# Kernel tuning notes

Measured on AMD Instinct MI355X. Metric: run time of the kernel, lower is better.

## Reference

```python
import jax, jax.numpy as jnp
import numpy as np

N_NODES = 30000
N_EDGES = 150000
N_REL = 10
IN_DIM = 256
OUT_DIM = 256


def setup_inputs() -> dict:
    key = jax.random.key(0)
    ks = jax.random.split(key, 10)
    s = 1.0 / np.sqrt(IN_DIM)  # ~nn.Linear init scale
    return {
        "x": jax.random.normal(ks[0], (N_NODES, IN_DIM), jnp.float32),
        "W_self": jax.random.uniform(ks[1], (IN_DIM, OUT_DIM), jnp.float32, -s, s),
        "b_self": jax.random.uniform(ks[2], (OUT_DIM,), jnp.float32, -s, s),
        "W_fwd": jax.random.uniform(ks[3], (N_REL, IN_DIM, OUT_DIM), jnp.float32, -s, s),
        "b_fwd": jax.random.uniform(ks[4], (N_REL, OUT_DIM), jnp.float32, -s, s),
        "W_rev": jax.random.uniform(ks[5], (N_REL, IN_DIM, OUT_DIM), jnp.float32, -s, s),
        "b_rev": jax.random.uniform(ks[6], (N_REL, OUT_DIM), jnp.float32, -s, s),
        "dep_idx": jax.random.randint(ks[7], (N_EDGES,), 0, N_NODES, jnp.int32),
        "rel_idx": jax.random.randint(ks[8], (N_EDGES,), 0, N_REL, jnp.int32),
        "gov_idx": jax.random.randint(ks[9], (N_EDGES,), 0, N_NODES, jnp.int32),
    }


def reference(x, W_self, b_self, W_fwd, b_fwd, W_rev, b_rev, dep_idx, rel_idx, gov_idx):
    # self transform for every token: [N, out]
    out = x @ W_self + b_self
    # transform all nodes by every relation weight up-front: [R, N, out]
    H_fwd = jnp.einsum("ni,rio->rno", x, W_fwd) + b_fwd[:, None, :]
    H_rev = jnp.einsum("ni,rio->rno", x, W_rev) + b_rev[:, None, :]
    # per-edge gather: forward msg uses governor feature, reverse msg uses dependent
    msg_fwd = H_fwd[rel_idx, gov_idx]  # [E, out]
    msg_rev = H_rev[rel_idx, dep_idx]  # [E, out]
    # scatter-add: forward msg -> dependent, reverse msg -> governor
    out = out.at[dep_idx].add(msg_fwd)
    out = out.at[gov_idx].add(msg_rev)
    return out
```

## Files before the change

kernel.cpp:

```cpp
#include <hip/hip_runtime.h>

#define N_NODES 30000
#define N_EDGES 150000
#define N_REL 10
#define DIM 256

#define SORT_BLOCKS 120
#define SORT_CHUNK ((N_EDGES + SORT_BLOCKS - 1) / SORT_BLOCKS)

#define SCAN_CHUNK 256
#define SCAN_BLOCKS ((N_NODES + SCAN_CHUNK - 1) / SCAN_CHUNK)

#define A_STRIDE 280

#define PREP_XB 7500
#define PREP_WB 5376
#define PREP_ZB 235

typedef __attribute__((ext_vector_type(8))) short bf16x8;
typedef __attribute__((ext_vector_type(4))) float f32x4;

__device__ __forceinline__ unsigned short f2bf(float f) {
  union { float f; unsigned int u; } v; v.f = f;
  unsigned int u = v.u;
  unsigned int r = u + 0x7fffu + ((u >> 16) & 1u);
  return (unsigned short)(r >> 16);
}


__global__ void prep_kernel(const float* __restrict__ x,
                            const float* __restrict__ Wf,
                            const float* __restrict__ Wr,
                            const float* __restrict__ Ws,
                            unsigned short* __restrict__ xbf,
                            unsigned short* __restrict__ wt,
                            int* __restrict__ cnt) {
  int b = blockIdx.x;
  if (b < PREP_XB) {
    int idx = b * 256 + threadIdx.x;
    float4 v = reinterpret_cast<const float4*>(x)[idx];
    ushort4 o;
    o.x = f2bf(v.x); o.y = f2bf(v.y); o.z = f2bf(v.z); o.w = f2bf(v.w);
    reinterpret_cast<ushort4*>(xbf)[idx] = o;
  } else if (b < PREP_XB + PREP_WB) {
    int idx = (b - PREP_XB) * 256 + threadIdx.x;
    int bb = idx >> 16;
    int t = idx & 65535;
    int o = t >> 8, i = t & 255;
    const float* src = (bb < N_REL) ? (Wf + (size_t)bb * 65536)
                     : (bb < 2 * N_REL) ? (Wr + (size_t)(bb - N_REL) * 65536)
                     : Ws;
    wt[idx] = f2bf(src[i * 256 + o]);
  } else {
    int i = (b - PREP_XB - PREP_WB) * 256 + threadIdx.x;
    if (i < 2 * N_NODES) cnt[i] = 0;
  }
}

__global__ void hist_all_kernel(const int* __restrict__ rel,
                                const int* __restrict__ dep,
                                const int* __restrict__ gov,
                                int* __restrict__ block_counts,
                                int* __restrict__ cnt) {
  __shared__ int h[N_REL];
  if (threadIdx.x < N_REL) h[threadIdx.x] = 0;
  __syncthreads();
  int beg = blockIdx.x * SORT_CHUNK;
  int end = min(beg + SORT_CHUNK, N_EDGES);
  for (int e = beg + threadIdx.x; e < end; e += blockDim.x) {
    atomicAdd(&h[rel[e]], 1);
    atomicAdd(&cnt[dep[e]], 1);
    atomicAdd(&cnt[N_NODES + gov[e]], 1);
  }
  __syncthreads();
  if (threadIdx.x < N_REL)
    block_counts[blockIdx.x * N_REL + threadIdx.x] = h[threadIdx.x];
}

__global__ void scan_rel_kernel(const int* __restrict__ block_counts,
                                int* __restrict__ rel_start,
                                int* __restrict__ block_offset) {
  __shared__ int tot[N_REL];
  int r = threadIdx.x;
  if (r < N_REL) {
    int s = 0;
    for (int b = 0; b < SORT_BLOCKS; ++b) s += block_counts[b * N_REL + r];
    tot[r] = s;
  }
  __syncthreads();
  if (threadIdx.x == 0) {
    int s = 0;
    for (int i = 0; i < N_REL; ++i) { rel_start[i] = s; s += tot[i]; }
    rel_start[N_REL] = s;
  }
  __syncthreads();
  if (r < N_REL) {
    int run = rel_start[r];
    for (int b = 0; b < SORT_BLOCKS; ++b) {
      block_offset[b * N_REL + r] = run;
      run += block_counts[b * N_REL + r];
    }
  }
}

__global__ void scanA_kernel(const int* __restrict__ cnt,
                             int* __restrict__ tmp, int* __restrict__ sums) {
  __shared__ int s[SCAN_CHUNK];
  int d = blockIdx.y, b = blockIdx.x, t = threadIdx.x;
  int i = b * SCAN_CHUNK + t;
  int v = (i < N_NODES) ? cnt[d * N_NODES + i] : 0;
  s[t] = v;
  __syncthreads();
  for (int off = 1; off < SCAN_CHUNK; off <<= 1) {
    int add = (t >= off) ? s[t - off] : 0;
    __syncthreads();
    s[t] += add;
    __syncthreads();
  }
  if (i < N_NODES) tmp[d * N_NODES + i] = s[t] - v;
  if (t == SCAN_CHUNK - 1) sums[d * SCAN_BLOCKS + b] = s[t];
}

__global__ void scanB_kernel(const int* __restrict__ sums,
                             int* __restrict__ chunk_off, int* __restrict__ rp) {
  __shared__ int s[128];
  int d = blockIdx.x, t = threadIdx.x;
  int v = (t < SCAN_BLOCKS) ? sums[d * SCAN_BLOCKS + t] : 0;
  s[t] = v;
  __syncthreads();
  for (int off = 1; off < 128; off <<= 1) {
    int add = (t >= off) ? s[t - off] : 0;
    __syncthreads();
    s[t] += add;
    __syncthreads();
  }
  if (t < SCAN_BLOCKS) chunk_off[d * SCAN_BLOCKS + t] = s[t] - v;
  if (t == 127) rp[d * (N_NODES + 1) + N_NODES] = s[127];
}

__global__ void scanC_kernel(const int* __restrict__ tmp,
                             const int* __restrict__ chunk_off,
                             int* __restrict__ rp, int* __restrict__ cursor) {
  int d = blockIdx.y;
  int i = blockIdx.x * SCAN_CHUNK + threadIdx.x;
  if (i < N_NODES) {
    int v = tmp[d * N_NODES + i] + chunk_off[d * SCAN_BLOCKS + blockIdx.x];
    rp[d * (N_NODES + 1) + i] = v;
    cursor[d * N_NODES + i] = v;
  }
}

__global__ void scatter_all_kernel(const int* __restrict__ rel,
                                   const int* __restrict__ dep,
                                   const int* __restrict__ gov,
                                   const int* __restrict__ block_offset,
                                   int* __restrict__ cursor,
                                   int* __restrict__ perm,
                                   int* __restrict__ srcf,
                                   int* __restrict__ srcr,
                                   int* __restrict__ colf,
                                   int* __restrict__ colr) {
  __shared__ int cur[N_REL];
  if (threadIdx.x < N_REL)
    cur[threadIdx.x] = block_offset[blockIdx.x * N_REL + threadIdx.x];
  __syncthreads();
  int beg = blockIdx.x * SORT_CHUNK;
  int end = min(beg + SORT_CHUNK, N_EDGES);
  for (int e = beg + threadIdx.x; e < end; e += blockDim.x) {
    int dp = dep[e], gv = gov[e];
    int pos = atomicAdd(&cur[rel[e]], 1);
    perm[pos] = e;
    srcf[pos] = gv;
    srcr[pos] = dp;
    colf[atomicAdd(&cursor[dp], 1)] = pos;
    colr[atomicAdd(&cursor[N_NODES + gv], 1)] = pos;
  }
}


__global__ __launch_bounds__(256, 2)
void mega_gemm_kernel(const unsigned short* __restrict__ xbf,
                      const unsigned short* __restrict__ wt,
                      const float* __restrict__ b_self,
                      const float* __restrict__ b_fwd,
                      const float* __restrict__ b_rev,
                      const int* __restrict__ srcf,
                      const int* __restrict__ srcr,
                      const int* __restrict__ rel_start,
                      unsigned short* __restrict__ msg,
                      float* __restrict__ out) {
  const int bkt = blockIdx.y;
  const bool is_self = (bkt >= 2 * N_REL);
  const bool fwd = bkt < N_REL;
  const int r = is_self ? 0 : (fwd ? bkt : bkt - N_REL);

  int beg, cnt;
  const int* src_arr = fwd ? srcf : srcr;
  unsigned short* mdir = msg + (fwd ? 0 : (size_t)N_EDGES * DIM);
  if (is_self) {
    beg = (bkt - 2 * N_REL) * (N_NODES / 2);
    cnt = N_NODES / 2;
  } else {
    beg = rel_start[r];
    cnt = rel_start[r + 1] - beg;
  }
  const int ntiles = (cnt + 63) >> 6;
  const int GX = gridDim.x;

  const int tid = threadIdx.x;
  const int wave = tid >> 6, lane = tid & 63;
  const int lm = lane & 15, q = lane >> 4;
  const int nb = wave * 64;
  const int half = lane >> 5;
  const int lcol = lane & 31;

  __shared__ int s_src[64];
  __shared__ unsigned short sA[64 * A_STRIDE];

  bf16x8 wf[8][4];
  const unsigned short* wbase = wt + (size_t)(is_self ? 2 * N_REL : bkt) * DIM * DIM;
  #pragma unroll
  for (int kk = 0; kk < 8; ++kk)
    #pragma unroll
    for (int ni = 0; ni < 4; ++ni)
      wf[kk][ni] = *reinterpret_cast<const bf16x8*>(
          wbase + (size_t)(nb + ni * 16 + lm) * DIM + kk * 32 + q * 8);

  const float* bptr = is_self ? b_self : ((fwd ? b_fwd : b_rev) + r * DIM);
  float bias[4];
  #pragma unroll
  for (int ni = 0; ni < 4; ++ni) bias[ni] = bptr[nb + ni * 16 + lm];

  int t = blockIdx.x;
  if (t >= ntiles) return;

  auto load_idx = [&](int tt) -> int {
    int tile0_ = tt << 6;
    if (is_self) {
      int rr = beg + tile0_ + tid;
      return rr < beg + cnt ? rr : beg + cnt - 1;
    } else {
      int p_ = tile0_ + tid;
      p_ = p_ < cnt ? p_ : cnt - 1;
      return src_arr[beg + p_];
    }
  };
  auto issue_D = [&](uint4* d) {
    #pragma unroll
    for (int i = 0; i < 8; ++i) {
      int row = wave * 16 + i * 2 + half;
      d[i] = *reinterpret_cast<const uint4*>(
          xbf + (size_t)s_src[row] * DIM + lcol * 8);
    }
  };
  auto write_A = [&](const uint4* d) {
    #pragma unroll
    for (int i = 0; i < 8; ++i) {
      int row = wave * 16 + i * 2 + half;
      *reinterpret_cast<uint4*>(sA + row * A_STRIDE + lcol * 8) = d[i];
    }
  };

  int idxreg = 0;
  if (tid < 64) s_src[tid] = load_idx(t);
  __syncthreads();
  uint4 d[8];
  issue_D(d);
  if (tid < 64 && t + GX < ntiles) idxreg = load_idx(t + GX);

  for (; t < ntiles; t += GX) {
    const int tile0 = t << 6;
    const int rows_valid = min(64, cnt - tile0);
    const bool have_next = (t + GX) < ntiles;
    const bool have_next2 = (t + 2 * GX) < ntiles;

    __syncthreads();
    if (tid < 64 && have_next) s_src[tid] = idxreg;
    write_A(d);
    if (tid < 64 && have_next2) idxreg = load_idx(t + 2 * GX);
    __syncthreads();
    if (have_next) issue_D(d);

    f32x4 acc[4][4];
    #pragma unroll
    for (int mi = 0; mi < 4; ++mi)
      #pragma unroll
      for (int ni = 0; ni < 4; ++ni)
        acc[mi][ni] = (f32x4){0.f, 0.f, 0.f, 0.f};

    #pragma unroll
    for (int kk = 0; kk < 8; ++kk) {
      bf16x8 a[4];
      #pragma unroll
      for (int mi = 0; mi < 4; ++mi)
        a[mi] = *reinterpret_cast<const bf16x8*>(
            sA + (mi * 16 + lm) * A_STRIDE + kk * 32 + q * 8);
      #pragma unroll
      for (int mi = 0; mi < 4; ++mi)
        #pragma unroll
        for (int ni = 0; ni < 4; ++ni)
          acc[mi][ni] = __builtin_amdgcn_mfma_f32_16x16x32_bf16(a[mi], wf[kk][ni], acc[mi][ni], 0, 0, 0);
    }

    if (is_self) {
      #pragma unroll
      for (int mi = 0; mi < 4; ++mi) {
        #pragma unroll
        for (int reg = 0; reg < 4; ++reg) {
          int row = mi * 16 + q * 4 + reg;
          if (row < rows_valid) {
            #pragma unroll
            for (int ni = 0; ni < 4; ++ni)
              out[(size_t)(beg + tile0 + row) * DIM + nb + ni * 16 + lm] =
                  acc[mi][ni][reg] + bias[ni];
          }
        }
      }
    } else {
      #pragma unroll
      for (int mi = 0; mi < 4; ++mi) {
        #pragma unroll
        for (int reg = 0; reg < 4; ++reg) {
          int row = mi * 16 + q * 4 + reg;
          if (row < rows_valid) {
            unsigned int p0 = ((unsigned int)f2bf(acc[mi][1][reg] + bias[1]) << 16) |
                              f2bf(acc[mi][0][reg] + bias[0]);
            unsigned int p1 = ((unsigned int)f2bf(acc[mi][3][reg] + bias[3]) << 16) |
                              f2bf(acc[mi][2][reg] + bias[2]);
            uint2 u; u.x = p0; u.y = p1;
            *reinterpret_cast<uint2*>(
                mdir + (size_t)(beg + tile0 + row) * DIM + nb + lm * 4) = u;
          }
        }
      }
    }
  }
}


__global__ void reduce_both_kernel(const unsigned short* __restrict__ msg,
                                   const int* __restrict__ rp,
                                   const int* __restrict__ colf,
                                   const int* __restrict__ colr,
                                   float* __restrict__ out) {
  const int n = blockIdx.x, t = threadIdx.x;
  const int g = t >> 6, lane = t & 63;
  const int b0 = rp[n], e0 = rp[n + 1];
  const int b1 = rp[(N_NODES + 1) + n], e1 = rp[(N_NODES + 1) + n + 1];
  if (e0 <= b0 && e1 <= b1) return;

  float a0 = 0.f, a1 = 0.f, a2 = 0.f, a3 = 0.f;
  for (int j = b0 + g; j < e0; j += 4) {
    int row = colf[j];
    uint2 v = *reinterpret_cast<const uint2*>(msg + (size_t)row * DIM + lane * 4);
    union { unsigned int u; float f; } c;
    c.u = v.x << 16;          a0 += c.f;
    c.u = v.x & 0xffff0000u;  a1 += c.f;
    c.u = v.y << 16;          a2 += c.f;
    c.u = v.y & 0xffff0000u;  a3 += c.f;
  }
  for (int j = b1 + g; j < e1; j += 4) {
    int row = colr[j];
    uint2 v = *reinterpret_cast<const uint2*>(
        msg + (size_t)(N_EDGES + row) * DIM + lane * 4);
    union { unsigned int u; float f; } c;
    c.u = v.x << 16;          a0 += c.f;
    c.u = v.x & 0xffff0000u;  a1 += c.f;
    c.u = v.y << 16;          a2 += c.f;
    c.u = v.y & 0xffff0000u;  a3 += c.f;
  }

  __shared__ float part[4][DIM];
  const int cb = (lane >> 4) * 64 + (lane & 15);
  part[g][cb +  0] = a0;
  part[g][cb + 16] = a1;
  part[g][cb + 32] = a2;
  part[g][cb + 48] = a3;
  __syncthreads();
  float s = part[0][t] + part[1][t] + part[2][t] + part[3][t];
  out[(size_t)n * DIM + t] += s;
}


__global__ __launch_bounds__(256, 2)
void self_gemm_kernel(const unsigned short* __restrict__ xbf,
                      const unsigned short* __restrict__ wt_self,
                      const float* __restrict__ b_self,
                      float* __restrict__ out) {
  const int tid = threadIdx.x;
  const int wave = tid >> 6, lane = tid & 63;
  const int lm = lane & 15, q = lane >> 4;
  const int nb = wave * 64;

  bf16x8 wf[8][4];
  #pragma unroll
  for (int kk = 0; kk < 8; ++kk)
    #pragma unroll
    for (int ni = 0; ni < 4; ++ni)
      wf[kk][ni] = *reinterpret_cast<const bf16x8*>(
          wt_self + (size_t)(nb + ni * 16 + lm) * DIM + kk * 32 + q * 8);

  float bias[4];
  #pragma unroll
  for (int ni = 0; ni < 4; ++ni) bias[ni] = b_self[nb + ni * 16 + lm];

  const int ntiles = (N_NODES + 63) / 64;
  for (int t = blockIdx.x; t < ntiles; t += gridDim.x) {
    const int row0 = t * 64;
    const unsigned short* xr[4];
    #pragma unroll
    for (int mi = 0; mi < 4; ++mi) {
      int r = row0 + mi * 16 + lm;
      int rc = r < N_NODES ? r : N_NODES - 1;
      xr[mi] = xbf + (size_t)rc * DIM + q * 8;
    }

    f32x4 acc[4][4];
    #pragma unroll
    for (int mi = 0; mi < 4; ++mi)
      #pragma unroll
      for (int ni = 0; ni < 4; ++ni)
        acc[mi][ni] = (f32x4){0.f, 0.f, 0.f, 0.f};

    #pragma unroll
    for (int kk = 0; kk < 8; ++kk) {
      bf16x8 a[4];
      #pragma unroll
      for (int mi = 0; mi < 4; ++mi)
        a[mi] = *reinterpret_cast<const bf16x8*>(xr[mi] + kk * 32);
      #pragma unroll
      for (int mi = 0; mi < 4; ++mi)
        #pragma unroll
        for (int ni = 0; ni < 4; ++ni)
          acc[mi][ni] = __builtin_amdgcn_mfma_f32_16x16x32_bf16(a[mi], wf[kk][ni], acc[mi][ni], 0, 0, 0);
    }

    #pragma unroll
    for (int mi = 0; mi < 4; ++mi) {
      #pragma unroll
      for (int reg = 0; reg < 4; ++reg) {
        int row = row0 + mi * 16 + q * 4 + reg;
        if (row < N_NODES) {
          #pragma unroll
          for (int ni = 0; ni < 4; ++ni)
            out[(size_t)row * DIM + nb + ni * 16 + lm] = acc[mi][ni][reg] + bias[ni];
        }
      }
    }
  }
}

__global__ void edge_gemm_atomic_kernel(const unsigned short* __restrict__ xbf,
                                        const unsigned short* __restrict__ wt,
                                        const float* __restrict__ b_fwd,
                                        const float* __restrict__ b_rev,
                                        const int* __restrict__ perm,
                                        const int* __restrict__ rel_start,
                                        const int* __restrict__ dep,
                                        const int* __restrict__ gov,
                                        float* __restrict__ out) {
  const int bucket = blockIdx.y;
  const int r = bucket % N_REL;
  const bool fwd = bucket < N_REL;
  const int beg = rel_start[r];
  const int cnt = rel_start[r + 1] - beg;
  const int ntiles = (cnt + 63) >> 6;

  const int tid = threadIdx.x;
  const int wave = tid >> 6, lane = tid & 63;
  const int lm = lane & 15, q = lane >> 4;
  const int nb = wave * 64;

  __shared__ int s_src[64], s_dst[64];

  const unsigned short* wr[4];
  #pragma unroll
  for (int ni = 0; ni < 4; ++ni)
    wr[ni] = wt + (size_t)bucket * DIM * DIM + (size_t)(nb + ni * 16 + lm) * DIM + q * 8;

  const float* bptr = (fwd ? b_fwd : b_rev) + r * DIM;
  float bias[4];
  #pragma unroll
  for (int ni = 0; ni < 4; ++ni) bias[ni] = bptr[nb + ni * 16 + lm];

  for (int t = blockIdx.x; t < ntiles; t += gridDim.x) {
    const int tile0 = t << 6;
    const int rows_valid = min(64, cnt - tile0);

    if (tid < 64) {
      int s = 0, d = -1;
      if (tid < rows_valid) {
        int e = perm[beg + tile0 + tid];
        int gv = gov[e], dp = dep[e];
        s = fwd ? gv : dp;
        d = fwd ? dp : gv;
      }
      s_src[tid] = s;
      s_dst[tid] = d;
    }
    __syncthreads();

    const unsigned short* xr[4];
    #pragma unroll
    for (int mi = 0; mi < 4; ++mi)
      xr[mi] = xbf + (size_t)s_src[mi * 16 + lm] * DIM + q * 8;

    f32x4 acc[4][4];
    #pragma unroll
    for (int mi = 0; mi < 4; ++mi)
      #pragma unroll
      for (int ni = 0; ni < 4; ++ni)
        acc[mi][ni] = (f32x4){0.f, 0.f, 0.f, 0.f};

    #pragma unroll
    for (int k0 = 0; k0 < DIM; k0 += 32) {
      bf16x8 a[4], b[4];
      #pragma unroll
      for (int mi = 0; mi < 4; ++mi) a[mi] = *reinterpret_cast<const bf16x8*>(xr[mi] + k0);
      #pragma unroll
      for (int ni = 0; ni < 4; ++ni) b[ni] = *reinterpret_cast<const bf16x8*>(wr[ni] + k0);
      #pragma unroll
      for (int mi = 0; mi < 4; ++mi)
        #pragma unroll
        for (int ni = 0; ni < 4; ++ni)
          acc[mi][ni] = __builtin_amdgcn_mfma_f32_16x16x32_bf16(a[mi], b[ni], acc[mi][ni], 0, 0, 0);
    }

    #pragma unroll
    for (int mi = 0; mi < 4; ++mi) {
      #pragma unroll
      for (int reg = 0; reg < 4; ++reg) {
        int row = mi * 16 + q * 4 + reg;
        if (row < rows_valid) {
          int dst = s_dst[row];
          float* op = out + (size_t)dst * DIM + nb + lm;
          #pragma unroll
          for (int ni = 0; ni < 4; ++ni)
            atomicAdd(op + ni * 16, acc[mi][ni][reg] + bias[ni]);
        }
      }
    }
    __syncthreads();
  }
}


extern "C" void kernel_launch(void* const* d_in, const int* in_sizes, int n_in,
                              void* d_out, int out_size, void* d_ws, size_t ws_size,
                              hipStream_t stream) {
  const float* x      = (const float*)d_in[0];
  const float* W_self = (const float*)d_in[1];
  const float* b_self = (const float*)d_in[2];
  const float* W_fwd  = (const float*)d_in[3];
  const float* b_fwd  = (const float*)d_in[4];
  const float* W_rev  = (const float*)d_in[5];
  const float* b_rev  = (const float*)d_in[6];
  const int* dep = (const int*)d_in[7];
  const int* rel = (const int*)d_in[8];
  const int* gov = (const int*)d_in[9];
  float* out = (float*)d_out;

  char* base = (char*)d_ws;
  size_t off = 0;
  auto alloc = [&](size_t bytes) -> char* {
    char* p = base + off;
    off = (off + bytes + 15) & ~(size_t)15;
    return p;
  };

  unsigned short* xbf = (unsigned short*)alloc((size_t)N_NODES * DIM * 2);
  unsigned short* wt  = (unsigned short*)alloc((size_t)21 * DIM * DIM * 2);
  int* perm          = (int*)alloc((size_t)N_EDGES * 4);
  int* srcf          = (int*)alloc((size_t)N_EDGES * 4);
  int* srcr          = (int*)alloc((size_t)N_EDGES * 4);
  int* rel_start     = (int*)alloc(16 * 4);
  int* block_counts  = (int*)alloc(SORT_BLOCKS * N_REL * 4);
  int* block_offset  = (int*)alloc(SORT_BLOCKS * N_REL * 4);
  int* cnt       = (int*)alloc((size_t)2 * N_NODES * 4);
  int* tmp       = (int*)alloc((size_t)2 * N_NODES * 4);
  int* sums      = (int*)alloc((size_t)2 * SCAN_BLOCKS * 4);
  int* chunk_off = (int*)alloc((size_t)2 * SCAN_BLOCKS * 4);
  int* rp        = (int*)alloc((size_t)2 * (N_NODES + 1) * 4);
  int* cursor    = (int*)alloc((size_t)2 * N_NODES * 4);
  int* colf      = (int*)alloc((size_t)N_EDGES * 4);
  int* colr      = (int*)alloc((size_t)N_EDGES * 4);
  unsigned short* msg = (unsigned short*)alloc((size_t)2 * N_EDGES * DIM * 2);
  const bool two_phase = (off <= ws_size);

  prep_kernel<<<PREP_XB + PREP_WB + PREP_ZB, 256, 0, stream>>>(
      x, W_fwd, W_rev, W_self, xbf, wt, cnt);
  hist_all_kernel<<<SORT_BLOCKS, 256, 0, stream>>>(rel, dep, gov, block_counts, cnt);
  scan_rel_kernel<<<1, 64, 0, stream>>>(block_counts, rel_start, block_offset);
  scanA_kernel<<<dim3(SCAN_BLOCKS, 2), SCAN_CHUNK, 0, stream>>>(cnt, tmp, sums);
  scanB_kernel<<<2, 128, 0, stream>>>(sums, chunk_off, rp);
  scanC_kernel<<<dim3(SCAN_BLOCKS, 2), SCAN_CHUNK, 0, stream>>>(tmp, chunk_off, rp, cursor);
  scatter_all_kernel<<<SORT_BLOCKS, 256, 0, stream>>>(
      rel, dep, gov, block_offset, cursor, perm, srcf, srcr, colf, colr);

  if (two_phase) {
    mega_gemm_kernel<<<dim3(48, 2 * N_REL + 2), 256, 0, stream>>>(
        xbf, wt, b_self, b_fwd, b_rev, srcf, srcr, rel_start, msg, out);
    reduce_both_kernel<<<N_NODES, 256, 0, stream>>>(msg, rp, colf, colr, out);
  } else {
    self_gemm_kernel<<<120, 256, 0, stream>>>(
        xbf, wt + (size_t)20 * DIM * DIM, b_self, out);
    edge_gemm_atomic_kernel<<<dim3(260, 20), 256, 0, stream>>>(
        xbf, wt, b_fwd, b_rev, perm, rel_start, dep, gov, out);
  }
}
```

Measured before the change: 323.7 us.

## Stream gathered rows straight into double-buffered swizzled LDS with global_load_lds

The gather of node feature rows into shared memory no longer passes through registers and a padded LDS tile. Rows are now loaded directly into LDS with global_load_lds, into a double-buffered tile using an XOR swizzle in place of padding to avoid bank conflicts. Staging of the next tile overlaps the MFMA work on the current one, and there is one fewer barrier per tile and fewer live registers. In exchange LDS use grows to about 64KB per block, which can lower occupancy, and correctness depends on the barrier waiting for the asynchronous LDS loads to finish.

```diff
diff --git a/kernel.cpp b/kernel.cpp
--- a/kernel.cpp
+++ b/kernel.cpp
@@ -10,8 +10,6 @@
 
 #define SCAN_CHUNK 256
 #define SCAN_BLOCKS ((N_NODES + SCAN_CHUNK - 1) / SCAN_CHUNK)
-
-#define A_STRIDE 280
 
 #define PREP_XB 7500
 #define PREP_WB 5376
@@ -212,13 +210,13 @@
   const int lm = lane & 15, q = lane >> 4;
   const int nb = wave * 64;
   const int half = lane >> 5;
-  const int lcol = lane & 31;
-
-  __shared__ int s_src[64];
-  __shared__ unsigned short sA[64 * A_STRIDE];
+
+  __shared__ int s_src[2][64];
+  __shared__ unsigned short sA[2][64 * DIM];
 
   bf16x8 wf[8][4];
-  const unsigned short* wbase = wt + (size_t)(is_self ? 2 * N_REL : bkt) * DIM * DIM;
+  const unsigned short* wbase =
+      wt + (size_t)(is_self ? 2 * N_REL : bkt) * DIM * DIM;
   #pragma unroll
   for (int kk = 0; kk < 8; ++kk)
     #pragma unroll
@@ -230,6 +228,18 @@
   float bias[4];
   #pragma unroll
   for (int ni = 0; ni < 4; ++ni) bias[ni] = bptr[nb + ni * 16 + lm];
+
+  int swz[8];
+  #pragma unroll
+  for (int i = 0; i < 8; ++i)
+    swz[i] = (((lane & 31) ^ ((i * 2 + half) & 7)) * 8);
+  int rowoff[4];
+  #pragma unroll
+  for (int mi = 0; mi < 4; ++mi) rowoff[mi] = (mi * 16 + lm) * DIM;
+  int ckoff[8];
+  #pragma unroll
+  for (int kk = 0; kk < 8; ++kk)
+    ckoff[kk] = ((kk * 4 + q) ^ (lm & 7)) * 8;
 
   int t = blockIdx.x;
   if (t >= ntiles) return;
@@ -245,41 +255,31 @@
       return src_arr[beg + p_];
     }
   };
-  auto issue_D = [&](uint4* d) {
+
+  auto issue_stage = [&](int p) {
+    const int* sp = s_src[p];
+    unsigned short* db = sA[p];
     #pragma unroll
     for (int i = 0; i < 8; ++i) {
-      int row = wave * 16 + i * 2 + half;
-      d[i] = *reinterpret_cast<const uint4*>(
-          xbf + (size_t)s_src[row] * DIM + lcol * 8);
+      int ldsrow = wave * 16 + i * 2;
+      int rr = sp[ldsrow + half];
+      const unsigned short* g = xbf + (size_t)rr * DIM + swz[i];
+      __builtin_amdgcn_global_load_lds(
+          (const __attribute__((address_space(1))) void*)g,
+          (__attribute__((address_space(3))) void*)(db + ldsrow * DIM),
+          16, 0, 0);
     }
   };
-  auto write_A = [&](const uint4* d) {
-    #pragma unroll
-    for (int i = 0; i < 8; ++i) {
-      int row = wave * 16 + i * 2 + half;
-      *reinterpret_cast<uint4*>(sA + row * A_STRIDE + lcol * 8) = d[i];
-    }
-  };
-
-  int idxreg = 0;
-  if (tid < 64) s_src[tid] = load_idx(t);
-  __syncthreads();
-  uint4 d[8];
-  issue_D(d);
-  if (tid < 64 && t + GX < ntiles) idxreg = load_idx(t + GX);
-
-  for (; t < ntiles; t += GX) {
+
+  auto step = [&](int cur) {
     const int tile0 = t << 6;
     const int rows_valid = min(64, cnt - tile0);
     const bool have_next = (t + GX) < ntiles;
     const bool have_next2 = (t + 2 * GX) < ntiles;
 
     __syncthreads();
-    if (tid < 64 && have_next) s_src[tid] = idxreg;
-    write_A(d);
-    if (tid < 64 && have_next2) idxreg = load_idx(t + 2 * GX);
-    __syncthreads();
-    if (have_next) issue_D(d);
+    if (have_next) issue_stage(cur ^ 1);
+    if (tid < 64 && have_next2) s_src[cur][tid] = load_idx(t + 2 * GX);
 
     f32x4 acc[4][4];
     #pragma unroll
@@ -288,18 +288,19 @@
       for (int ni = 0; ni < 4; ++ni)
         acc[mi][ni] = (f32x4){0.f, 0.f, 0.f, 0.f};
 
+    const unsigned short* sAb = sA[cur];
     #pragma unroll
     for (int kk = 0; kk < 8; ++kk) {
       bf16x8 a[4];
       #pragma unroll
       for (int mi = 0; mi < 4; ++mi)
-        a[mi] = *reinterpret_cast<const bf16x8*>(
-            sA + (mi * 16 + lm) * A_STRIDE + kk * 32 + q * 8);
+        a[mi] = *reinterpret_cast<const bf16x8*>(sAb + rowoff[mi] + ckoff[kk]);
       #pragma unroll
       for (int mi = 0; mi < 4; ++mi)
         #pragma unroll
         for (int ni = 0; ni < 4; ++ni)
-          acc[mi][ni] = __builtin_amdgcn_mfma_f32_16x16x32_bf16(a[mi], wf[kk][ni], acc[mi][ni], 0, 0, 0);
+          acc[mi][ni] = __builtin_amdgcn_mfma_f32_16x16x32_bf16(
+              a[mi], wf[kk][ni], acc[mi][ni], 0, 0, 0);
     }
 
     if (is_self) {
@@ -334,6 +335,18 @@
         }
       }
     }
+  };
+
+  if (tid < 64) s_src[0][tid] = load_idx(t);
+  __syncthreads();
+  issue_stage(0);
+  if (tid < 64 && t + GX < ntiles) s_src[1][tid] = load_idx(t + GX);
+
+  while (true) {
+    step(0);
+    t += GX; if (t >= ntiles) break;
+    step(1);
+    t += GX; if (t >= ntiles) break;
   }
 }
 
```

Result: faster. 288.3 us (-10.9%).
